# Kernel optimization log

Measured on AMD Instinct MI355X. Metric: run time of the kernel, lower is better.

The kernel has to match this reference:

```python
import jax, jax.numpy as jnp
import numpy as np

DIM = 768
NUM_HEADS = 12
HEAD_DIM = DIM // NUM_HEADS
ORDER_H = 8
RENORM = True
B, N = 4, 1024


def setup_inputs() -> dict:
    key = jax.random.key(0)
    ks = jax.random.split(key, 8)
    return {
        "x": jax.random.normal(ks[0], (B, N, DIM), dtype=jnp.float32),
        "qkv_w": jax.random.normal(ks[1], (3 * DIM, DIM), dtype=jnp.float32) * (DIM ** -0.5),
        "qkv_b": jax.random.normal(ks[2], (3 * DIM,), dtype=jnp.float32) * 0.02,
        "proj_w": jax.random.normal(ks[3], (DIM, DIM), dtype=jnp.float32) * (DIM ** -0.5),
        "proj_b": jax.random.normal(ks[4], (DIM,), dtype=jnp.float32) * 0.02,
        "lamb": jax.random.normal(ks[5], (NUM_HEADS,), dtype=jnp.float32) * 0.1,
        "gamma": 1.0 + jax.random.normal(ks[6], (NUM_HEADS,), dtype=jnp.float32) * 0.1,
        "delta": jax.random.normal(ks[7], (NUM_HEADS,), dtype=jnp.float32) * 0.1,
    }


def reference(x, qkv_w, qkv_b, proj_w, proj_b, lamb, gamma, delta):
    Bx, Nx, C = x.shape
    scale = HEAD_DIM ** -0.5
    # qkv: [B,N,3C] -> [3,B,H,N,hd]
    qkv = (x @ qkv_w.T + qkv_b).reshape(Bx, Nx, 3, NUM_HEADS, HEAD_DIM)
    qkv = jnp.transpose(qkv, (2, 0, 3, 1, 4))
    q, k, v = qkv[0], qkv[1], qkv[2]
    attn = jax.nn.softmax(jnp.einsum("bhid,bhjd->bhij", q, k) * scale, axis=-1)
    I = jnp.eye(Nx, dtype=attn.dtype)
    # GFSA high-order term: (h-1)*(A - I)@A + A
    high = (ORDER_H - 1) * jnp.einsum("bhik,bhkj->bhij", attn - I, attn) + attn
    beta_ = lamb[None, :, None, None]
    gamma_ = gamma[None, :, None, None]
    delta_ = delta[None, :, None, None]
    attn = delta_ * I + gamma_ * attn + beta_ * high
    if RENORM:
        attn = jnp.maximum(attn, 0.0)
        attn = attn / (attn.sum(axis=-1, keepdims=True) + 1e-9)
    out = jnp.einsum("bhij,bhjd->bhid", attn, v)  # [B,H,N,hd]
    out = jnp.transpose(out, (0, 2, 1, 3)).reshape(Bx, Nx, C)
    return out @ proj_w.T + proj_b
```

## Files before the change

kernel.cpp:

```cpp
#include <hip/hip_runtime.h>
#include <hip/hip_bf16.h>

#define DIMC 768
#define NH 12
#define HD 64
#define BB 4
#define NN 1024
#define BHT 48
#define QKVC 2304

typedef unsigned short u16;
typedef __attribute__((ext_vector_type(4))) unsigned short u16x4;
typedef __attribute__((ext_vector_type(8))) unsigned short u16x8;
typedef __attribute__((ext_vector_type(8))) short s16x8;
typedef __attribute__((ext_vector_type(4))) float f32x4;

#define GLD16(g, l) __builtin_amdgcn_global_load_lds( \
    (__attribute__((address_space(1))) void*)(g),     \
    (__attribute__((address_space(3))) void*)(l), 16, 0, 0)

__device__ __forceinline__ u16 f2bf(float f) {
    unsigned u = __float_as_uint(f);
    return (u16)((u + 0x7FFF + ((u >> 16) & 1)) >> 16);
}
__device__ __forceinline__ float bf2f(u16 v) {
    return __uint_as_float(((unsigned)v) << 16);
}
struct bfp { u16 h, l; };
__device__ __forceinline__ bfp splitf(float f) {
    bfp r;
    r.h = f2bf(f);
    r.l = f2bf(f - bf2f(r.h));
    return r;
}

__device__ __forceinline__ int swz_linear() {
    const int nwg = gridDim.x * gridDim.y * gridDim.z;
    const int L = blockIdx.x + gridDim.x * (blockIdx.y + gridDim.y * blockIdx.z);
    return (L & 7) * (nwg >> 3) + (L >> 3);
}

__global__ __launch_bounds__(256) void split_f2b(
    const float* __restrict__ src, u16* __restrict__ hi, u16* __restrict__ lo,
    int n4)
{
    int idx = blockIdx.x * 256 + threadIdx.x;
    if (idx >= n4) return;
    float4 v = *(const float4*)&src[idx * 4];
    u16x4 h, l;
    bfp s;
    s = splitf(v.x); h[0] = s.h; l[0] = s.l;
    s = splitf(v.y); h[1] = s.h; l[1] = s.l;
    s = splitf(v.z); h[2] = s.h; l[2] = s.l;
    s = splitf(v.w); h[3] = s.h; l[3] = s.l;
    *(u16x4*)&hi[idx * 4] = h;
    *(u16x4*)&lo[idx * 4] = l;
}

__global__ __launch_bounds__(256) void gemm3_mfma(
    int Mrows, int Nout, int K,
    const u16* __restrict__ Ahp, const u16* __restrict__ Alp,
    const u16* __restrict__ Bhp, const u16* __restrict__ Blp,
    const float* __restrict__ bias, float* __restrict__ C)
{
    __shared__ alignas(16) u16 sAh[128 * 32], sAl[128 * 32], sBh[128 * 32], sBl[128 * 32];
    const int tid = threadIdx.x;
    const int W = swz_linear();
    const int j0 = (W % gridDim.x) * 128, i0 = (W / gridDim.x) * 128;
    const int w = tid >> 6, l = tid & 63;
    const int wr = w >> 1, wc = w & 1;
    const int l15 = l & 15, kb4 = l >> 4;
    const int lrow = l >> 2, lch = (l & 3) * 8;

    f32x4 acc[4][4];
    const f32x4 zero = {0.f, 0.f, 0.f, 0.f};
#pragma unroll
    for (int a = 0; a < 4; ++a)
#pragma unroll
        for (int b = 0; b < 4; ++b) acc[a][b] = zero;

    for (int k0 = 0; k0 < K; k0 += 32) {
#pragma unroll
        for (int t = 0; t < 2; ++t) {
            const int r = w * 32 + t * 16;
            const size_t ar = (size_t)(i0 + r + lrow) * K + k0 + lch;
            const size_t br = (size_t)(j0 + r + lrow) * K + k0 + lch;
            GLD16(&Ahp[ar], &sAh[r * 32]);
            GLD16(&Alp[ar], &sAl[r * 32]);
            GLD16(&Bhp[br], &sBh[r * 32]);
            GLD16(&Blp[br], &sBl[r * 32]);
        }
        __syncthreads();

        s16x8 ah[4], al[4], bh[4], bl[4];
#pragma unroll
        for (int f = 0; f < 4; ++f) {
            const int ao = (wr * 64 + f * 16 + l15) * 32 + kb4 * 8;
            const int bo = (wc * 64 + f * 16 + l15) * 32 + kb4 * 8;
            ah[f] = *(const s16x8*)&sAh[ao];
            al[f] = *(const s16x8*)&sAl[ao];
            bh[f] = *(const s16x8*)&sBh[bo];
            bl[f] = *(const s16x8*)&sBl[bo];
        }
#pragma unroll
        for (int fr = 0; fr < 4; ++fr)
#pragma unroll
            for (int fc = 0; fc < 4; ++fc) {
                acc[fr][fc] = __builtin_amdgcn_mfma_f32_16x16x32_bf16(
                    ah[fr], bh[fc], acc[fr][fc], 0, 0, 0);
                acc[fr][fc] = __builtin_amdgcn_mfma_f32_16x16x32_bf16(
                    ah[fr], bl[fc], acc[fr][fc], 0, 0, 0);
                acc[fr][fc] = __builtin_amdgcn_mfma_f32_16x16x32_bf16(
                    al[fr], bh[fc], acc[fr][fc], 0, 0, 0);
            }
        __syncthreads();
    }

#pragma unroll
    for (int fr = 0; fr < 4; ++fr)
#pragma unroll
        for (int r = 0; r < 4; ++r) {
            const int gi = i0 + wr * 64 + fr * 16 + kb4 * 4 + r;
#pragma unroll
            for (int fc = 0; fc < 4; ++fc) {
                const int gj = j0 + wc * 64 + fc * 16 + l15;
                C[(size_t)gi * Nout + gj] = acc[fr][fc][r] + bias[gj];
            }
        }
}

__global__ __launch_bounds__(256) void qkv_fused_mfma(
    const u16* __restrict__ Ahp, const u16* __restrict__ Alp,
    const u16* __restrict__ Bhp, const u16* __restrict__ Blp,
    const float* __restrict__ bias,
    u16* __restrict__ qh, u16* __restrict__ ql,
    u16* __restrict__ kh, u16* __restrict__ kl,
    u16* __restrict__ vth, u16* __restrict__ vtl)
{
    __shared__ alignas(16) u16 sAh[128 * 32], sAl[128 * 32], sBh[128 * 32], sBl[128 * 32];
    const int tid = threadIdx.x;
    const int W = swz_linear();
    const int j0 = (W % gridDim.x) * 128, i0 = (W / gridDim.x) * 128;
    const int w = tid >> 6, l = tid & 63;
    const int wr = w >> 1, wc = w & 1;
    const int l15 = l & 15, kb4 = l >> 4;
    const int lrow = l >> 2, lch = (l & 3) * 8;
    const int K = DIMC;

    f32x4 acc[4][4];
    const f32x4 zero = {0.f, 0.f, 0.f, 0.f};
#pragma unroll
    for (int a = 0; a < 4; ++a)
#pragma unroll
        for (int b = 0; b < 4; ++b) acc[a][b] = zero;

    for (int k0 = 0; k0 < K; k0 += 32) {
#pragma unroll
        for (int t = 0; t < 2; ++t) {
            const int r = w * 32 + t * 16;
            const size_t ar = (size_t)(i0 + r + lrow) * K + k0 + lch;
            const size_t br = (size_t)(j0 + r + lrow) * K + k0 + lch;
            GLD16(&Ahp[ar], &sAh[r * 32]);
            GLD16(&Alp[ar], &sAl[r * 32]);
            GLD16(&Bhp[br], &sBh[r * 32]);
            GLD16(&Blp[br], &sBl[r * 32]);
        }
        __syncthreads();

        s16x8 ah[4], al[4], bh[4], bl[4];
#pragma unroll
        for (int f = 0; f < 4; ++f) {
            const int ao = (wr * 64 + f * 16 + l15) * 32 + kb4 * 8;
            const int bo = (wc * 64 + f * 16 + l15) * 32 + kb4 * 8;
            ah[f] = *(const s16x8*)&sAh[ao];
            al[f] = *(const s16x8*)&sAl[ao];
            bh[f] = *(const s16x8*)&sBh[bo];
            bl[f] = *(const s16x8*)&sBl[bo];
        }
#pragma unroll
        for (int fr = 0; fr < 4; ++fr)
#pragma unroll
            for (int fc = 0; fc < 4; ++fc) {
                acc[fr][fc] = __builtin_amdgcn_mfma_f32_16x16x32_bf16(
                    ah[fr], bh[fc], acc[fr][fc], 0, 0, 0);
                acc[fr][fc] = __builtin_amdgcn_mfma_f32_16x16x32_bf16(
                    ah[fr], bl[fc], acc[fr][fc], 0, 0, 0);
                acc[fr][fc] = __builtin_amdgcn_mfma_f32_16x16x32_bf16(
                    al[fr], bh[fc], acc[fr][fc], 0, 0, 0);
            }
        __syncthreads();
    }

    const int part = j0 / DIMC;
    const int hbase = (j0 % DIMC) >> 6;
    const int h = hbase + wc;

#pragma unroll
    for (int fr = 0; fr < 4; ++fr) {
        const int rowbase = i0 + wr * 64 + fr * 16 + kb4 * 4;
        const int b = rowbase >> 10;
        const int n0 = rowbase & 1023;
        const int bh = b * NH + h;
#pragma unroll
        for (int fc = 0; fc < 4; ++fc) {
            const int gj = j0 + wc * 64 + fc * 16 + l15;
            const float bv = bias[gj];
            const int d = fc * 16 + l15;
            if (part == 0) {
#pragma unroll
                for (int r = 0; r < 4; ++r) {
                    bfp s = splitf((acc[fr][fc][r] + bv) * 0.125f);
                    const size_t o = ((size_t)bh * NN + n0 + r) * HD + d;
                    qh[o] = s.h; ql[o] = s.l;
                }
            } else if (part == 1) {
#pragma unroll
                for (int r = 0; r < 4; ++r) {
                    bfp s = splitf(acc[fr][fc][r] + bv);
                    const size_t o = ((size_t)bh * NN + n0 + r) * HD + d;
                    kh[o] = s.h; kl[o] = s.l;
                }
            } else {
                u16x4 hv, lv;
#pragma unroll
                for (int r = 0; r < 4; ++r) {
                    bfp s = splitf(acc[fr][fc][r] + bv);
                    hv[r] = s.h; lv[r] = s.l;
                }
                const size_t o = ((size_t)bh * HD + d) * NN + n0;
                *(u16x4*)&vth[o] = hv;
                *(u16x4*)&vtl[o] = lv;
            }
        }
    }
}

__global__ __launch_bounds__(256) void qk_mfma(
    const u16* __restrict__ qh, const u16* __restrict__ ql,
    const u16* __restrict__ kh, const u16* __restrict__ kl,
    float* __restrict__ Sb, int h0)
{
    __shared__ alignas(16) u16 sAh[128 * 32], sAl[128 * 32], sBh[128 * 32], sBl[128 * 32];
    const int tid = threadIdx.x;
    const int W = swz_linear();
    const int bhl = W >> 6;
    const int ib = W & 63;
    const int j0 = (ib & 7) * 128, i0 = (ib >> 3) * 128;
    const int bh = h0 + bhl;
    const int w = tid >> 6, l = tid & 63;
    const int wr = w >> 1, wc = w & 1;
    const int l15 = l & 15, kb4 = l >> 4;
    const int lrow = l >> 2, lch = (l & 3) * 8;

    f32x4 acc[4][4];
    const f32x4 zero = {0.f, 0.f, 0.f, 0.f};
#pragma unroll
    for (int a = 0; a < 4; ++a)
#pragma unroll
        for (int b = 0; b < 4; ++b) acc[a][b] = zero;

    for (int k0 = 0; k0 < HD; k0 += 32) {
#pragma unroll
        for (int t = 0; t < 2; ++t) {
            const int r = w * 32 + t * 16;
            const size_t ar = ((size_t)bh * NN + i0 + r + lrow) * HD + k0 + lch;
            const size_t br = ((size_t)bh * NN + j0 + r + lrow) * HD + k0 + lch;
            GLD16(&qh[ar], &sAh[r * 32]);
            GLD16(&ql[ar], &sAl[r * 32]);
            GLD16(&kh[br], &sBh[r * 32]);
            GLD16(&kl[br], &sBl[r * 32]);
        }
        __syncthreads();

        s16x8 ah[4], al[4], bh[4], bl[4];
#pragma unroll
        for (int f = 0; f < 4; ++f) {
            const int ao = (wr * 64 + f * 16 + l15) * 32 + kb4 * 8;
            const int bo = (wc * 64 + f * 16 + l15) * 32 + kb4 * 8;
            ah[f] = *(const s16x8*)&sAh[ao];
            al[f] = *(const s16x8*)&sAl[ao];
            bh[f] = *(const s16x8*)&sBh[bo];
            bl[f] = *(const s16x8*)&sBl[bo];
        }
#pragma unroll
        for (int fr = 0; fr < 4; ++fr)
#pragma unroll
            for (int fc = 0; fc < 4; ++fc) {
                acc[fr][fc] = __builtin_amdgcn_mfma_f32_16x16x32_bf16(
                    ah[fr], bh[fc], acc[fr][fc], 0, 0, 0);
                acc[fr][fc] = __builtin_amdgcn_mfma_f32_16x16x32_bf16(
                    ah[fr], bl[fc], acc[fr][fc], 0, 0, 0);
                acc[fr][fc] = __builtin_amdgcn_mfma_f32_16x16x32_bf16(
                    al[fr], bh[fc], acc[fr][fc], 0, 0, 0);
            }
        __syncthreads();
    }

    float* Sh = Sb + (size_t)bhl * NN * NN;
#pragma unroll
    for (int fr = 0; fr < 4; ++fr)
#pragma unroll
        for (int r = 0; r < 4; ++r) {
            const int gi = i0 + wr * 64 + fr * 16 + kb4 * 4 + r;
#pragma unroll
            for (int fc = 0; fc < 4; ++fc) {
                const int gj = j0 + wc * 64 + fc * 16 + l15;
                Sh[(size_t)gi * NN + gj] = acc[fr][fc][r];
            }
        }
}

__global__ __launch_bounds__(256) void softmax_b(
    const float* __restrict__ Sb, u16* __restrict__ Abf)
{
    const int row = blockIdx.x;
    const float* p = Sb + (size_t)row * NN;
    u16* q = Abf + (size_t)row * NN;
    const int tid = threadIdx.x;
    __shared__ float redm[4], reds[4];

    float4 v = *(const float4*)&p[tid * 4];
    float m = fmaxf(fmaxf(v.x, v.y), fmaxf(v.z, v.w));
#pragma unroll
    for (int off = 32; off >= 1; off >>= 1) m = fmaxf(m, __shfl_xor(m, off));
    if ((tid & 63) == 0) redm[tid >> 6] = m;
    __syncthreads();
    m = fmaxf(fmaxf(redm[0], redm[1]), fmaxf(redm[2], redm[3]));

    v.x = expf(v.x - m); v.y = expf(v.y - m);
    v.z = expf(v.z - m); v.w = expf(v.w - m);
    float s = v.x + v.y + v.z + v.w;
#pragma unroll
    for (int off = 32; off >= 1; off >>= 1) s += __shfl_xor(s, off);
    if ((tid & 63) == 0) reds[tid >> 6] = s;
    __syncthreads();
    s = reds[0] + reds[1] + reds[2] + reds[3];

    const float inv = 1.0f / s;
    u16x4 o;
    o[0] = f2bf(v.x * inv); o[1] = f2bf(v.y * inv);
    o[2] = f2bf(v.z * inv); o[3] = f2bf(v.w * inv);
    *(u16x4*)&q[tid * 4] = o;
}

__global__ __launch_bounds__(256) void mpow_mfma(
    const u16* __restrict__ Abf, u16* __restrict__ Mb,
    const float* __restrict__ lamb, const float* __restrict__ gamma,
    const float* __restrict__ delta, int h0)
{
    __shared__ alignas(16) u16 sA[128 * 32], sB[128 * 32];
    const int tid = threadIdx.x;
    const int W = swz_linear();
    const int bz = W >> 6;
    const int ib = W & 63;
    const int j0 = (ib & 7) * 128, i0 = (ib >> 3) * 128;
    const int h = (h0 + bz) % NH;
    const u16* Ah = Abf + (size_t)bz * NN * NN;

    const int w = tid >> 6, l = tid & 63;
    const int wr = w >> 1, wc = w & 1;
    const int l15 = l & 15, kb4 = l >> 4;
    const int lrow = l >> 2, lch = (l & 3) * 8;
    const int kr = tid & 31;
    const int jc = (tid >> 5) * 16;

    f32x4 acc[4][4];
    const f32x4 zero = {0.f, 0.f, 0.f, 0.f};
#pragma unroll
    for (int a = 0; a < 4; ++a)
#pragma unroll
        for (int b = 0; b < 4; ++b) acc[a][b] = zero;

    for (int k0 = 0; k0 < NN; k0 += 32) {
#pragma unroll
        for (int t = 0; t < 2; ++t) {
            const int r = w * 32 + t * 16;
            GLD16(&Ah[(size_t)(i0 + r + lrow) * NN + k0 + lch], &sA[r * 32]);
        }
        {
            const u16* arow = &Ah[(size_t)(k0 + kr) * NN + j0 + jc];
            u16x8 b0 = *(const u16x8*)arow;
            u16x8 b1 = *(const u16x8*)(arow + 8);
#pragma unroll
            for (int e = 0; e < 8; ++e) {
                const int j1 = jc + e;
                const int j2 = jc + 8 + e;
                sB[(j1 ^ ((j1 >> 4) & 1)) * 32 + kr] = b0[e];
                sB[(j2 ^ ((j2 >> 4) & 1)) * 32 + kr] = b1[e];
            }
        }
        __syncthreads();

        s16x8 af[4], bf[4];
#pragma unroll
        for (int f = 0; f < 4; ++f) {
            af[f] = *(const s16x8*)&sA[(wr * 64 + f * 16 + l15) * 32 + kb4 * 8];
            const int jrow = wc * 64 + f * 16 + l15;
            const int jphys = jrow ^ ((jrow >> 4) & 1);
            bf[f] = *(const s16x8*)&sB[jphys * 32 + kb4 * 8];
        }
#pragma unroll
        for (int fr = 0; fr < 4; ++fr)
#pragma unroll
            for (int fc = 0; fc < 4; ++fc)
                acc[fr][fc] = __builtin_amdgcn_mfma_f32_16x16x32_bf16(
                    af[fr], bf[fc], acc[fr][fc], 0, 0, 0);
        __syncthreads();
    }

    const float lam = lamb[h];
    const float c1 = gamma[h] - 6.0f * lam;
    const float c2 = 7.0f * lam;
    const float del = delta[h];
    u16* Mh = Mb + (size_t)bz * NN * NN;

#pragma unroll
    for (int fr = 0; fr < 4; ++fr)
#pragma unroll
        for (int r = 0; r < 4; ++r) {
            const int gi = i0 + wr * 64 + fr * 16 + kb4 * 4 + r;
#pragma unroll
            for (int fc = 0; fc < 4; ++fc) {
                const int gj = j0 + wc * 64 + fc * 16 + l15;
                const float a = bf2f(Ah[(size_t)gi * NN + gj]);
                float m = c2 * acc[fr][fc][r] + c1 * a + (gi == gj ? del : 0.f);
                m = fmaxf(m, 0.f);
                Mh[(size_t)gi * NN + gj] = f2bf(m);
            }
        }
}

__global__ __launch_bounds__(256) void pv_mfma(
    const u16* __restrict__ Mb,
    const u16* __restrict__ vth, const u16* __restrict__ vtl,
    u16* __restrict__ aoh, u16* __restrict__ aol, int h0)
{
    __shared__ alignas(16) u16 sM[128 * 32], sVh[64 * 32], sVl[64 * 32];
    const int tid = threadIdx.x;
    const int W = swz_linear();
    const int bhl = W >> 3;
    const int i0 = (W & 7) * 128;
    const int bh = h0 + bhl;
    const int b = bh / NH, h = bh % NH;
    const u16* Mh = Mb + (size_t)bhl * NN * NN;
    const u16* vhb = vth + (size_t)bh * HD * NN;
    const u16* vlb = vtl + (size_t)bh * HD * NN;

    const int w = tid >> 6, l = tid & 63;
    const int l15 = l & 15, kb4 = l >> 4;
    const int lrow = l >> 2, lch = (l & 3) * 8;

    f32x4 acc[2][4], accs[2];
    const f32x4 zero = {0.f, 0.f, 0.f, 0.f};
#pragma unroll
    for (int a = 0; a < 2; ++a) {
#pragma unroll
        for (int c = 0; c < 4; ++c) acc[a][c] = zero;
        accs[a] = zero;
    }
    s16x8 ones;
#pragma unroll
    for (int e = 0; e < 8; ++e) ones[e] = (short)0x3F80;

    for (int k0 = 0; k0 < NN; k0 += 32) {
#pragma unroll
        for (int t = 0; t < 2; ++t) {
            const int r = w * 32 + t * 16;
            GLD16(&Mh[(size_t)(i0 + r + lrow) * NN + k0 + lch], &sM[r * 32]);
        }
        {
            const int r = w * 16;
            const size_t vr = (size_t)(r + lrow) * NN + k0 + lch;
            GLD16(&vhb[vr], &sVh[r * 32]);
            GLD16(&vlb[vr], &sVl[r * 32]);
        }
        __syncthreads();

        s16x8 af[2], bh[4], bl[4];
#pragma unroll
        for (int f = 0; f < 2; ++f)
            af[f] = *(const s16x8*)&sM[(w * 32 + f * 16 + l15) * 32 + kb4 * 8];
#pragma unroll
        for (int f = 0; f < 4; ++f) {
            bh[f] = *(const s16x8*)&sVh[(f * 16 + l15) * 32 + kb4 * 8];
            bl[f] = *(const s16x8*)&sVl[(f * 16 + l15) * 32 + kb4 * 8];
        }
#pragma unroll
        for (int fr = 0; fr < 2; ++fr) {
#pragma unroll
            for (int fc = 0; fc < 4; ++fc) {
                acc[fr][fc] = __builtin_amdgcn_mfma_f32_16x16x32_bf16(
                    af[fr], bh[fc], acc[fr][fc], 0, 0, 0);
                acc[fr][fc] = __builtin_amdgcn_mfma_f32_16x16x32_bf16(
                    af[fr], bl[fc], acc[fr][fc], 0, 0, 0);
            }
            accs[fr] = __builtin_amdgcn_mfma_f32_16x16x32_bf16(
                af[fr], ones, accs[fr], 0, 0, 0);
        }
        __syncthreads();
    }

#pragma unroll
    for (int fr = 0; fr < 2; ++fr)
#pragma unroll
        for (int r = 0; r < 4; ++r) {
            const int gi = i0 + w * 32 + fr * 16 + kb4 * 4 + r;
            const float inv = 1.0f / (accs[fr][r] + 1e-9f);
            const size_t ob = (size_t)(b * NN + gi) * DIMC + h * HD;
#pragma unroll
            for (int fc = 0; fc < 4; ++fc) {
                const int gd = fc * 16 + l15;
                bfp s = splitf(acc[fr][fc][r] * inv);
                aoh[ob + gd] = s.h;
                aol[ob + gd] = s.l;
            }
        }
}

extern "C" void kernel_launch(void* const* d_in, const int* in_sizes, int n_in,
                              void* d_out, int out_size, void* d_ws, size_t ws_size,
                              hipStream_t stream)
{
    const float* x      = (const float*)d_in[0];
    const float* qkv_w  = (const float*)d_in[1];
    const float* qkv_b  = (const float*)d_in[2];
    const float* proj_w = (const float*)d_in[3];
    const float* proj_b = (const float*)d_in[4];
    const float* lamb   = (const float*)d_in[5];
    const float* gamma  = (const float*)d_in[6];
    const float* delta  = (const float*)d_in[7];

    char* p = (char*)d_ws;
    u16* xh  = (u16*)p;                     p += (size_t)4096 * DIMC * 2;
    u16* xl  = (u16*)p;                     p += (size_t)4096 * DIMC * 2;
    u16* wh  = (u16*)p;                     p += (size_t)QKVC * DIMC * 2;
    u16* wl  = (u16*)p;                     p += (size_t)QKVC * DIMC * 2;
    u16* pwh = (u16*)p;                     p += (size_t)DIMC * DIMC * 2;
    u16* pwl = (u16*)p;                     p += (size_t)DIMC * DIMC * 2;
    u16* qh  = (u16*)p;                     p += (size_t)BHT * NN * HD * 2;
    u16* ql  = (u16*)p;                     p += (size_t)BHT * NN * HD * 2;
    u16* kh  = (u16*)p;                     p += (size_t)BHT * NN * HD * 2;
    u16* kl  = (u16*)p;                     p += (size_t)BHT * NN * HD * 2;
    u16* vth = (u16*)p;                     p += (size_t)BHT * HD * NN * 2;
    u16* vtl = (u16*)p;                     p += (size_t)BHT * HD * NN * 2;
    u16* aoh = (u16*)p;                     p += (size_t)4096 * DIMC * 2;
    u16* aol = (u16*)p;                     p += (size_t)4096 * DIMC * 2;
    const size_t fixed = (size_t)(p - (char*)d_ws);

    const size_t perh = (size_t)NN * NN * 4 + (size_t)NN * NN * 2;
    static const int choices[] = {48, 24, 16, 12, 8, 6, 4, 3, 2, 1};
    int CH = 1;
    for (int ci = 0; ci < 10; ++ci) {
        int c = choices[ci];
        if (fixed + (size_t)c * perh <= ws_size) { CH = c; break; }
    }

    float* Sb = (float*)p;                  p += (size_t)CH * NN * NN * 4;
    u16* Abf  = (u16*)p;                    p += (size_t)CH * NN * NN * 2;
    u16* Mb   = (u16*)Sb;

    split_f2b<<<dim3((4096 * DIMC / 4 + 255) / 256), 256, 0, stream>>>(x, xh, xl, 4096 * DIMC / 4);
    split_f2b<<<dim3((QKVC * DIMC / 4 + 255) / 256), 256, 0, stream>>>(qkv_w, wh, wl, QKVC * DIMC / 4);
    split_f2b<<<dim3((DIMC * DIMC / 4 + 255) / 256), 256, 0, stream>>>(proj_w, pwh, pwl, DIMC * DIMC / 4);

    qkv_fused_mfma<<<dim3(QKVC / 128, 4096 / 128), 256, 0, stream>>>(
        xh, xl, wh, wl, qkv_b, qh, ql, kh, kl, vth, vtl);

    for (int h0 = 0; h0 < BHT; h0 += CH) {
        qk_mfma<<<dim3(8, 8, CH), 256, 0, stream>>>(qh, ql, kh, kl, Sb, h0);
        softmax_b<<<dim3(CH * NN), 256, 0, stream>>>(Sb, Abf);
        mpow_mfma<<<dim3(8, 8, CH), 256, 0, stream>>>(
            Abf, Mb, lamb, gamma, delta, h0);
        pv_mfma<<<dim3(8, CH), 256, 0, stream>>>(Mb, vth, vtl, aoh, aol, h0);
    }

    gemm3_mfma<<<dim3(DIMC / 128, 4096 / 128), 256, 0, stream>>>(
        4096, DIMC, DIMC, aoh, aol, pwh, pwl, proj_b, (float*)d_out);
}
```

Before: 448.6 us.

## Use wave-per-row softmax and XOR-swizzle LDS tiles in matrix-power kernel

The softmax kernel now gives each 64-lane wave one full row, so it reduces with shuffles alone and drops the shared-memory reductions and block barriers. Each block handles four rows. Separately, the mpow kernel's A and B LDS tiles switch from a row-level XOR to an 8-element chunk-level XOR swizzle applied on both the global-to-LDS loads and the fragment reads. This is meant to reduce LDS bank conflicts on the 16-byte fragment loads. The risk is that the swizzle must match exactly between writer and reader, and the scalar B-tile stores may still conflict.

```diff
diff --git a/kernel.cpp b/kernel.cpp
--- a/kernel.cpp
+++ b/kernel.cpp
@@ -310,37 +310,42 @@
         }
 }
 
-__global__ __launch_bounds__(256) void softmax_b(
+__global__ __launch_bounds__(256) void softmax_w(
     const float* __restrict__ Sb, u16* __restrict__ Abf)
 {
-    const int row = blockIdx.x;
+    const int w = threadIdx.x >> 6, l = threadIdx.x & 63;
+    const int row = blockIdx.x * 4 + w;
     const float* p = Sb + (size_t)row * NN;
     u16* q = Abf + (size_t)row * NN;
-    const int tid = threadIdx.x;
-    __shared__ float redm[4], reds[4];
-
-    float4 v = *(const float4*)&p[tid * 4];
-    float m = fmaxf(fmaxf(v.x, v.y), fmaxf(v.z, v.w));
+
+    float4 v[4];
+    float m = -1e30f;
+#pragma unroll
+    for (int c = 0; c < 4; ++c) {
+        v[c] = *(const float4*)&p[c * 256 + l * 4];
+        m = fmaxf(m, fmaxf(fmaxf(v[c].x, v[c].y), fmaxf(v[c].z, v[c].w)));
+    }
 #pragma unroll
     for (int off = 32; off >= 1; off >>= 1) m = fmaxf(m, __shfl_xor(m, off));
-    if ((tid & 63) == 0) redm[tid >> 6] = m;
-    __syncthreads();
-    m = fmaxf(fmaxf(redm[0], redm[1]), fmaxf(redm[2], redm[3]));
-
-    v.x = expf(v.x - m); v.y = expf(v.y - m);
-    v.z = expf(v.z - m); v.w = expf(v.w - m);
-    float s = v.x + v.y + v.z + v.w;
+
+    float s = 0.f;
+#pragma unroll
+    for (int c = 0; c < 4; ++c) {
+        v[c].x = expf(v[c].x - m); v[c].y = expf(v[c].y - m);
+        v[c].z = expf(v[c].z - m); v[c].w = expf(v[c].w - m);
+        s += v[c].x + v[c].y + v[c].z + v[c].w;
+    }
 #pragma unroll
     for (int off = 32; off >= 1; off >>= 1) s += __shfl_xor(s, off);
-    if ((tid & 63) == 0) reds[tid >> 6] = s;
-    __syncthreads();
-    s = reds[0] + reds[1] + reds[2] + reds[3];
 
     const float inv = 1.0f / s;
-    u16x4 o;
-    o[0] = f2bf(v.x * inv); o[1] = f2bf(v.y * inv);
-    o[2] = f2bf(v.z * inv); o[3] = f2bf(v.w * inv);
-    *(u16x4*)&q[tid * 4] = o;
+#pragma unroll
+    for (int c = 0; c < 4; ++c) {
+        u16x4 o;
+        o[0] = f2bf(v[c].x * inv); o[1] = f2bf(v[c].y * inv);
+        o[2] = f2bf(v[c].z * inv); o[3] = f2bf(v[c].w * inv);
+        *(u16x4*)&q[c * 256 + l * 4] = o;
+    }
 }
 
 __global__ __launch_bounds__(256) void mpow_mfma(
@@ -360,9 +365,12 @@
     const int w = tid >> 6, l = tid & 63;
     const int wr = w >> 1, wc = w & 1;
     const int l15 = l & 15, kb4 = l >> 4;
-    const int lrow = l >> 2, lch = (l & 3) * 8;
+    const int lrow = l >> 2;
+    const int lchz = (((l & 3) ^ ((lrow >> 1) & 3)) * 8);
+    const int swf = (l15 >> 1) & 3;
     const int kr = tid & 31;
     const int jc = (tid >> 5) * 16;
+    const int krc = kr >> 3, kri = kr & 7;
 
     f32x4 acc[4][4];
     const f32x4 zero = {0.f, 0.f, 0.f, 0.f};
@@ -375,7 +383,7 @@
 #pragma unroll
         for (int t = 0; t < 2; ++t) {
             const int r = w * 32 + t * 16;
-            GLD16(&Ah[(size_t)(i0 + r + lrow) * NN + k0 + lch], &sA[r * 32]);
+            GLD16(&Ah[(size_t)(i0 + r + lrow) * NN + k0 + lchz], &sA[r * 32]);
         }
         {
             const u16* arow = &Ah[(size_t)(k0 + kr) * NN + j0 + jc];
@@ -385,8 +393,8 @@
             for (int e = 0; e < 8; ++e) {
                 const int j1 = jc + e;
                 const int j2 = jc + 8 + e;
-                sB[(j1 ^ ((j1 >> 4) & 1)) * 32 + kr] = b0[e];
-                sB[(j2 ^ ((j2 >> 4) & 1)) * 32 + kr] = b1[e];
+                sB[j1 * 32 + ((krc ^ ((j1 >> 1) & 3)) * 8) + kri] = b0[e];
+                sB[j2 * 32 + ((krc ^ ((j2 >> 1) & 3)) * 8) + kri] = b1[e];
             }
         }
         __syncthreads();
@@ -394,10 +402,9 @@
         s16x8 af[4], bf[4];
 #pragma unroll
         for (int f = 0; f < 4; ++f) {
-            af[f] = *(const s16x8*)&sA[(wr * 64 + f * 16 + l15) * 32 + kb4 * 8];
-            const int jrow = wc * 64 + f * 16 + l15;
-            const int jphys = jrow ^ ((jrow >> 4) & 1);
-            bf[f] = *(const s16x8*)&sB[jphys * 32 + kb4 * 8];
+            const int co = (kb4 ^ swf) * 8;
+            af[f] = *(const s16x8*)&sA[(wr * 64 + f * 16 + l15) * 32 + co];
+            bf[f] = *(const s16x8*)&sB[(wc * 64 + f * 16 + l15) * 32 + co];
         }
 #pragma unroll
         for (int fr = 0; fr < 4; ++fr)
@@ -568,7 +575,7 @@
 
     for (int h0 = 0; h0 < BHT; h0 += CH) {
         qk_mfma<<<dim3(8, 8, CH), 256, 0, stream>>>(qh, ql, kh, kl, Sb, h0);
-        softmax_b<<<dim3(CH * NN), 256, 0, stream>>>(Sb, Abf);
+        softmax_w<<<dim3(CH * NN / 4), 256, 0, stream>>>(Sb, Abf);
         mpow_mfma<<<dim3(8, 8, CH), 256, 0, stream>>>(
             Abf, Mb, lamb, gamma, delta, h0);
         pv_mfma<<<dim3(8, CH), 256, 0, stream>>>(Mb, vth, vtl, aoh, aol, h0);
```

Measured after the change: 432.4 us. -3.6%, faster.
